# Kernel tuning notes

Hardware: AMD Instinct MI355X
Metric: run time of the kernel (lower is better)

## Reference

```python
import jax, jax.numpy as jnp
import numpy as np

QUERY_DIM = 1024
KEY_DIM = 768
NUM_HEADS = 16
HEAD_DIM = QUERY_DIM // NUM_HEADS
SCALE = HEAD_DIM ** -0.5


def setup_inputs() -> dict:
    key = jax.random.key(0)
    ks = jax.random.split(key, 11)
    B, Nq, Nk = 4, 4096, 1024
    s_q = QUERY_DIM ** -0.5
    s_k = KEY_DIM ** -0.5
    return {
        "query": jax.random.normal(ks[0], (B, Nq, QUERY_DIM), jnp.float32),
        "key": jax.random.normal(ks[1], (B, Nk, KEY_DIM), jnp.float32),
        "value": jax.random.normal(ks[2], (B, Nk, KEY_DIM), jnp.float32),
        "Wq": jax.random.normal(ks[3], (QUERY_DIM, QUERY_DIM), jnp.float32) * s_q,
        "bq": jnp.zeros((QUERY_DIM,), jnp.float32),
        "Wk": jax.random.normal(ks[4], (KEY_DIM, QUERY_DIM), jnp.float32) * s_k,
        "bk": jnp.zeros((QUERY_DIM,), jnp.float32),
        "Wv": jax.random.normal(ks[5], (KEY_DIM, QUERY_DIM), jnp.float32) * s_k,
        "bv": jnp.zeros((QUERY_DIM,), jnp.float32),
        "Wo": jax.random.normal(ks[6], (QUERY_DIM, QUERY_DIM), jnp.float32) * s_q,
        "bo": jnp.zeros((QUERY_DIM,), jnp.float32),
    }


def reference(query, key, value, Wq, bq, Wk, bk, Wv, bv, Wo, bo):
    B, Nq, _ = query.shape
    Nk = key.shape[1]
    # projections to (B, H, N, d)
    q = (query @ Wq + bq).reshape(B, Nq, NUM_HEADS, HEAD_DIM).transpose(0, 2, 1, 3)
    k = (key @ Wk + bk).reshape(B, Nk, NUM_HEADS, HEAD_DIM).transpose(0, 2, 1, 3)
    v = (value @ Wv + bv).reshape(B, Nk, NUM_HEADS, HEAD_DIM).transpose(0, 2, 1, 3)
    attn = jnp.einsum("bhqd,bhkd->bhqk", q, k) * SCALE
    attn = jax.nn.softmax(attn, axis=-1)
    out = jnp.einsum("bhqk,bhkd->bhqd", attn, v)
    out = out.transpose(0, 2, 1, 3).reshape(B, Nq, QUERY_DIM)
    return out @ Wo + bo
```

## Files before the change

### kernel.cpp

```cpp
#include <hip/hip_runtime.h>
#include <hip/hip_bf16.h>
#include <stdint.h>


typedef unsigned short u16;
typedef __attribute__((ext_vector_type(8))) short short8;
typedef __attribute__((ext_vector_type(4))) float f32x4;

#define B_SZ 4
#define NQ   4096
#define NK   1024
#define QDIM 1024
#define KDIM 768
#define NH   16
#define HD   64
#define QSCALE (0.125f * 1.44269504f)

__device__ __forceinline__ u16 f2bf(float f) {
  union { float f; uint32_t u; } v; v.f = f;
  uint32_t u = v.u;
  return (u16)((u + 0x7FFFu + ((u >> 16) & 1u)) >> 16);
}

__device__ __forceinline__ uint32_t pk2(float a, float b) {
  union { __hip_bfloat162 h; uint32_t u; } cv;
  cv.h = __float22bfloat162_rn(float2{a, b});
  return cv.u;
}

__device__ __forceinline__ float fexp2(float x) {
  return __builtin_amdgcn_exp2f(x);
}

__device__ __forceinline__ void async16(u16* lds, const u16* g) {
  __builtin_amdgcn_global_load_lds(
      (__attribute__((address_space(1))) void*)(g),
      (__attribute__((address_space(3))) void*)(lds), 16, 0, 0);
}

__global__ __launch_bounds__(256) void f32_to_bf16_k(const float* __restrict__ in,
                                                     u16* __restrict__ out, int n4) {
  int i = blockIdx.x * 256 + threadIdx.x;
  if (i < n4) {
    f32x4 v = ((const f32x4*)in)[i];
    uint2 o = {pk2(v.x, v.y), pk2(v.z, v.w)};
    ((uint2*)out)[i] = o;
  }
}

__global__ __launch_bounds__(256) void f32_to_bf16_2k(const float* __restrict__ a,
                                                      const float* __restrict__ b,
                                                      u16* __restrict__ oa,
                                                      u16* __restrict__ ob, int n4) {
  int i = blockIdx.x * 256 + threadIdx.x;
  const float* in = blockIdx.y ? b : a;
  u16* out = blockIdx.y ? ob : oa;
  if (i < n4) {
    f32x4 v = ((const f32x4*)in)[i];
    uint2 o = {pk2(v.x, v.y), pk2(v.z, v.w)};
    ((uint2*)out)[i] = o;
  }
}

__global__ __launch_bounds__(256) void transpose_bf16_k(const float* __restrict__ W,
                                                        u16* __restrict__ Wt,
                                                        int K, int N) {
  __shared__ float t[32][33];
  int tx = threadIdx.x & 31, ty = threadIdx.x >> 5;
  int nb = blockIdx.x * 32, kb = blockIdx.y * 32;
#pragma unroll
  for (int i = 0; i < 4; ++i)
    t[ty + i * 8][tx] = W[(size_t)(kb + ty + i * 8) * N + nb + tx];
  __syncthreads();
#pragma unroll
  for (int i = 0; i < 4; ++i)
    Wt[(size_t)(nb + ty + i * 8) * K + kb + tx] = f2bf(t[tx][ty + i * 8]);
}

__global__ __launch_bounds__(256) void gemm_bt(const u16* __restrict__ A,
                                               const u16* __restrict__ Bt,
                                               const float* __restrict__ bias,
                                               float* __restrict__ Cf,
                                               u16* __restrict__ Cb,
                                               int M, int N, int K, int out_bf16,
                                               float scale) {
  __shared__ __align__(16) u16 Al[128 * 64];
  __shared__ __align__(16) u16 Bl[128 * 64];
  const int tid = threadIdx.x;
  const int w = tid >> 6, lane = tid & 63;
  const int g = lane >> 4, l15 = lane & 15;
  const int sw = l15 & 7;
  const int mbase = blockIdx.x * 128, nbase = blockIdx.y * 128;
  const int wm = (w & 1) * 64, wn = (w >> 1) * 64;

  f32x4 zero4 = {0.f, 0.f, 0.f, 0.f};
  f32x4 acc[4][4];
#pragma unroll
  for (int i = 0; i < 4; ++i)
#pragma unroll
    for (int j = 0; j < 4; ++j) acc[i][j] = zero4;

  for (int kb = 0; kb < K; kb += 64) {
#pragma unroll
    for (int i = 0; i < 4; ++i) {
      int cbase = w * 256 + i * 64;
      int c = cbase + lane;
      int row = c >> 3;
      int kc8 = ((c & 7) ^ (row & 7)) * 8;
      async16(&Al[cbase * 8], A + (size_t)(mbase + row) * K + kb + kc8);
      async16(&Bl[cbase * 8], Bt + (size_t)(nbase + row) * K + kb + kc8);
    }
    __syncthreads();
#pragma unroll
    for (int ks = 0; ks < 2; ++ks) {
      short8 af[4], bf[4];
#pragma unroll
      for (int mt = 0; mt < 4; ++mt)
        af[mt] = *(const short8*)&Al[(wm + mt * 16 + l15) * 64 + ((ks * 4 + g) ^ sw) * 8];
#pragma unroll
      for (int nt = 0; nt < 4; ++nt)
        bf[nt] = *(const short8*)&Bl[(wn + nt * 16 + l15) * 64 + ((ks * 4 + g) ^ sw) * 8];
#pragma unroll
      for (int mt = 0; mt < 4; ++mt)
#pragma unroll
        for (int nt = 0; nt < 4; ++nt)
          acc[mt][nt] = __builtin_amdgcn_mfma_f32_16x16x32_bf16(af[mt], bf[nt],
                                                                acc[mt][nt], 0, 0, 0);
    }
    __syncthreads();
  }

#pragma unroll
  for (int nt = 0; nt < 4; ++nt) {
    int col = nbase + wn + nt * 16 + l15;
    float bv = bias[col];
#pragma unroll
    for (int mt = 0; mt < 4; ++mt)
#pragma unroll
      for (int r = 0; r < 4; ++r) {
        int row = mbase + wm + mt * 16 + g * 4 + r;
        float v = (acc[mt][nt][r] + bv) * scale;
        if (out_bf16) Cb[(size_t)row * N + col] = f2bf(v);
        else          Cf[(size_t)row * N + col] = v;
      }
  }
}

__global__ __launch_bounds__(256) void gemm_kv(const u16* __restrict__ kA,
                                               const u16* __restrict__ vA,
                                               const u16* __restrict__ Wk,
                                               const u16* __restrict__ Wv,
                                               const float* __restrict__ bk,
                                               const float* __restrict__ bv,
                                               u16* __restrict__ Kp,
                                               u16* __restrict__ VT,
                                               int M, int N, int K) {
  __shared__ __align__(16) u16 Al[128 * 64];
  __shared__ __align__(16) u16 Bl[128 * 64];
  const int ct = blockIdx.z;
  const u16* A  = ct ? vA : kA;
  const u16* Bt = ct ? Wv : Wk;
  const float* bias = ct ? bv : bk;
  const int tid = threadIdx.x;
  const int w = tid >> 6, lane = tid & 63;
  const int g = lane >> 4, l15 = lane & 15;
  const int sw = l15 & 7;
  const int mbase = blockIdx.x * 128, nbase = blockIdx.y * 128;
  const int wm = (w & 1) * 64, wn = (w >> 1) * 64;

  f32x4 zero4 = {0.f, 0.f, 0.f, 0.f};
  f32x4 acc[4][4];
#pragma unroll
  for (int i = 0; i < 4; ++i)
#pragma unroll
    for (int j = 0; j < 4; ++j) acc[i][j] = zero4;

  for (int kb = 0; kb < K; kb += 64) {
#pragma unroll
    for (int i = 0; i < 4; ++i) {
      int cbase = w * 256 + i * 64;
      int c = cbase + lane;
      int row = c >> 3;
      int kc8 = ((c & 7) ^ (row & 7)) * 8;
      async16(&Al[cbase * 8], A + (size_t)(mbase + row) * K + kb + kc8);
      async16(&Bl[cbase * 8], Bt + (size_t)(nbase + row) * K + kb + kc8);
    }
    __syncthreads();
#pragma unroll
    for (int ks = 0; ks < 2; ++ks) {
      short8 af[4], bf[4];
#pragma unroll
      for (int mt = 0; mt < 4; ++mt)
        af[mt] = *(const short8*)&Al[(wm + mt * 16 + l15) * 64 + ((ks * 4 + g) ^ sw) * 8];
#pragma unroll
      for (int nt = 0; nt < 4; ++nt)
        bf[nt] = *(const short8*)&Bl[(wn + nt * 16 + l15) * 64 + ((ks * 4 + g) ^ sw) * 8];
      if (ct) {
#pragma unroll
        for (int nt = 0; nt < 4; ++nt)
#pragma unroll
          for (int mt = 0; mt < 4; ++mt)
            acc[nt][mt] = __builtin_amdgcn_mfma_f32_16x16x32_bf16(bf[nt], af[mt],
                                                                  acc[nt][mt], 0, 0, 0);
      } else {
#pragma unroll
        for (int mt = 0; mt < 4; ++mt)
#pragma unroll
          for (int nt = 0; nt < 4; ++nt)
            acc[mt][nt] = __builtin_amdgcn_mfma_f32_16x16x32_bf16(af[mt], bf[nt],
                                                                  acc[mt][nt], 0, 0, 0);
      }
    }
    __syncthreads();
  }

  if (ct) {
#pragma unroll
    for (int mt = 0; mt < 4; ++mt) {
      int m = mbase + wm + mt * 16 + l15;
#pragma unroll
      for (int nt = 0; nt < 4; ++nt)
#pragma unroll
        for (int r = 0; r < 4; ++r) {
          int n = nbase + wn + nt * 16 + g * 4 + r;
          VT[(size_t)n * M + m] = f2bf(acc[nt][mt][r] + bias[n]);
        }
    }
  } else {
#pragma unroll
    for (int nt = 0; nt < 4; ++nt) {
      int col = nbase + wn + nt * 16 + l15;
      float bvv = bias[col];
#pragma unroll
      for (int mt = 0; mt < 4; ++mt)
#pragma unroll
        for (int r = 0; r < 4; ++r) {
          int row = mbase + wm + mt * 16 + g * 4 + r;
          Kp[(size_t)row * N + col] = f2bf(acc[mt][nt][r] + bvv);
        }
    }
  }
}

__global__ __launch_bounds__(256, 2) void attn_kernel(const u16* __restrict__ Qp,
                                                      const u16* __restrict__ Kp,
                                                      const u16* __restrict__ VT,
                                                      u16* __restrict__ AO) {
  __shared__ __align__(16) u16 K_lds[2][64 * 64];
  __shared__ __align__(16) u16 V_lds[3][64 * 64];
  __shared__ __align__(16) u16 P_lds[4][32 * 64];

  const int tid = threadIdx.x;
  const int w = tid >> 6, lane = tid & 63;
  const int g = lane >> 4, l15 = lane & 15;
  const int sw = l15 & 7;
  const int bh = blockIdx.y, b = bh >> 4, h = bh & 15;
  const int qrow0 = blockIdx.x * 128 + w * 32;
  const int MT = B_SZ * NK;

  const int cbase0 = (w * 2 + 0) * 64;
  const int cbase1 = (w * 2 + 1) * 64;
  const int c0 = cbase0 + lane, c1 = cbase1 + lane;
  const int row0 = c0 >> 3, kc80 = ((c0 & 7) ^ (row0 & 7)) * 8;
  const int row1 = c1 >> 3, kc81 = ((c1 & 7) ^ (row1 & 7)) * 8;

  const u16* kp0 = Kp + (size_t)(b * NK + row0) * QDIM + h * HD + kc80;
  const u16* kp1 = Kp + (size_t)(b * NK + row1) * QDIM + h * HD + kc81;
  const u16* vp0 = VT + (size_t)(h * HD + row0) * MT + b * NK + kc80;
  const u16* vp1 = VT + (size_t)(h * HD + row1) * MT + b * NK + kc81;

  const int rb = l15 * 64;
  const int cs0 = (g ^ sw) * 8;
  const int cs1 = ((4 + g) ^ sw) * 8;
  const int pwb = rb + (((g >> 1) ^ (sw & 1)) * 8) + (g & 1) * 4;
  const int pms = sw & 6;

  short8 ones8;
#pragma unroll
  for (int j = 0; j < 8; ++j) ones8[j] = (short)0x3F80;

  short8 qf[2][2];
#pragma unroll
  for (int qt = 0; qt < 2; ++qt)
#pragma unroll
    for (int ks = 0; ks < 2; ++ks) {
      size_t row = (size_t)(b * NQ + qrow0 + qt * 16 + l15);
      qf[qt][ks] = *(const short8*)(Qp + row * QDIM + h * HD + ks * 32 + g * 8);
    }

  f32x4 zero4 = {0.f, 0.f, 0.f, 0.f};
  f32x4 o4[4][2];
  f32x4 lacc[2];
#pragma unroll
  for (int dt = 0; dt < 4; ++dt)
#pragma unroll
    for (int qt = 0; qt < 2; ++qt) o4[dt][qt] = zero4;
  lacc[0] = zero4; lacc[1] = zero4;

  u16* Pl = &P_lds[w][0];

  async16(&K_lds[0][cbase0 * 8], kp0);
  async16(&K_lds[0][cbase1 * 8], kp1);
  async16(&V_lds[0][cbase0 * 8], vp0);
  async16(&V_lds[0][cbase1 * 8], vp1);
  kp0 += 64 * QDIM; kp1 += 64 * QDIM; vp0 += 64; vp1 += 64;
  __syncthreads();

  async16(&K_lds[1][cbase0 * 8], kp0);
  async16(&K_lds[1][cbase1 * 8], kp1);
  async16(&V_lds[1][cbase0 * 8], vp0);
  async16(&V_lds[1][cbase1 * 8], vp1);
  kp0 += 64 * QDIM; kp1 += 64 * QDIM; vp0 += 64; vp1 += 64;

  {
    const u16* Kl = &K_lds[0][0];
    f32x4 sc[4][2];
    short8 kf0[4], kf1[4];
#pragma unroll
    for (int mt = 0; mt < 4; ++mt) {
      kf0[mt] = *(const short8*)&Kl[mt * 1024 + rb + cs0];
      kf1[mt] = *(const short8*)&Kl[mt * 1024 + rb + cs1];
    }
    __builtin_amdgcn_s_setprio(1);
#pragma unroll
    for (int mt = 0; mt < 4; ++mt)
#pragma unroll
      for (int qt = 0; qt < 2; ++qt)
        sc[mt][qt] = __builtin_amdgcn_mfma_f32_16x16x32_bf16(kf0[mt], qf[qt][0],
                                                             zero4, 0, 0, 0);
#pragma unroll
    for (int mt = 0; mt < 4; ++mt)
#pragma unroll
      for (int qt = 0; qt < 2; ++qt)
        sc[mt][qt] = __builtin_amdgcn_mfma_f32_16x16x32_bf16(kf1[mt], qf[qt][1],
                                                             sc[mt][qt], 0, 0, 0);
    __builtin_amdgcn_s_setprio(0);
#pragma unroll
    for (int qt = 0; qt < 2; ++qt)
#pragma unroll
      for (int mt = 0; mt < 4; ++mt) {
        float p0 = fexp2(sc[mt][qt][0]);
        float p1 = fexp2(sc[mt][qt][1]);
        float p2 = fexp2(sc[mt][qt][2]);
        float p3 = fexp2(sc[mt][qt][3]);
        uint2 pk = {pk2(p0, p1), pk2(p2, p3)};
        *(uint2*)&Pl[qt * 1024 + pwb + ((mt * 2) ^ pms) * 8] = pk;
      }
  }
  __syncthreads();

  for (int kc = 1; kc < NK / 64; ++kc) {
    const int pv = (kc - 1) % 3;
    if (kc + 1 < NK / 64) {
      const int nk = (kc + 1) & 1, nv = (kc + 1) % 3;
      async16(&K_lds[nk][cbase0 * 8], kp0);
      async16(&K_lds[nk][cbase1 * 8], kp1);
      async16(&V_lds[nv][cbase0 * 8], vp0);
      async16(&V_lds[nv][cbase1 * 8], vp1);
      kp0 += 64 * QDIM; kp1 += 64 * QDIM; vp0 += 64; vp1 += 64;
    }
    const u16* Kl = &K_lds[kc & 1][0];
    const u16* Vl = &V_lds[pv][0];

    short8 pb[2][2], vf[2][4], kf[2][4];
#pragma unroll
    for (int qt = 0; qt < 2; ++qt) {
      pb[0][qt] = *(const short8*)&Pl[qt * 1024 + rb + cs0];
      pb[1][qt] = *(const short8*)&Pl[qt * 1024 + rb + cs1];
    }
#pragma unroll
    for (int dt = 0; dt < 4; ++dt) {
      vf[0][dt] = *(const short8*)&Vl[dt * 1024 + rb + cs0];
      vf[1][dt] = *(const short8*)&Vl[dt * 1024 + rb + cs1];
    }
#pragma unroll
    for (int mt = 0; mt < 4; ++mt) {
      kf[0][mt] = *(const short8*)&Kl[mt * 1024 + rb + cs0];
      kf[1][mt] = *(const short8*)&Kl[mt * 1024 + rb + cs1];
    }

    f32x4 sc[4][2];
    __builtin_amdgcn_s_setprio(1);
#pragma unroll
    for (int mt = 0; mt < 4; ++mt)
#pragma unroll
      for (int qt = 0; qt < 2; ++qt)
        sc[mt][qt] = __builtin_amdgcn_mfma_f32_16x16x32_bf16(kf[0][mt], qf[qt][0],
                                                             zero4, 0, 0, 0);
#pragma unroll
    for (int qt = 0; qt < 2; ++qt)
      lacc[qt] = __builtin_amdgcn_mfma_f32_16x16x32_bf16(ones8, pb[0][qt],
                                                         lacc[qt], 0, 0, 0);
#pragma unroll
    for (int dt = 0; dt < 4; ++dt)
#pragma unroll
      for (int qt = 0; qt < 2; ++qt)
        o4[dt][qt] = __builtin_amdgcn_mfma_f32_16x16x32_bf16(vf[0][dt], pb[0][qt],
                                                             o4[dt][qt], 0, 0, 0);
#pragma unroll
    for (int mt = 0; mt < 4; ++mt)
#pragma unroll
      for (int qt = 0; qt < 2; ++qt)
        sc[mt][qt] = __builtin_amdgcn_mfma_f32_16x16x32_bf16(kf[1][mt], qf[qt][1],
                                                             sc[mt][qt], 0, 0, 0);
#pragma unroll
    for (int qt = 0; qt < 2; ++qt)
      lacc[qt] = __builtin_amdgcn_mfma_f32_16x16x32_bf16(ones8, pb[1][qt],
                                                         lacc[qt], 0, 0, 0);
#pragma unroll
    for (int dt = 0; dt < 4; ++dt)
#pragma unroll
      for (int qt = 0; qt < 2; ++qt)
        o4[dt][qt] = __builtin_amdgcn_mfma_f32_16x16x32_bf16(vf[1][dt], pb[1][qt],
                                                             o4[dt][qt], 0, 0, 0);
    __builtin_amdgcn_s_setprio(0);

#pragma unroll
    for (int qt = 0; qt < 2; ++qt)
#pragma unroll
      for (int mt = 0; mt < 4; ++mt) {
        float p0 = fexp2(sc[mt][qt][0]);
        float p1 = fexp2(sc[mt][qt][1]);
        float p2 = fexp2(sc[mt][qt][2]);
        float p3 = fexp2(sc[mt][qt][3]);
        uint2 pk = {pk2(p0, p1), pk2(p2, p3)};
        *(uint2*)&Pl[qt * 1024 + pwb + ((mt * 2) ^ pms) * 8] = pk;
      }

    asm volatile("s_waitcnt vmcnt(2)" ::: "memory");
    __builtin_amdgcn_sched_barrier(0);
    __builtin_amdgcn_s_barrier();
  }

  asm volatile("s_waitcnt vmcnt(0)" ::: "memory");
  __builtin_amdgcn_sched_barrier(0);
  __builtin_amdgcn_s_barrier();

  {
    const u16* Vl = &V_lds[(NK / 64 - 1) % 3][0];
    short8 pb[2][2], vf[2][4];
#pragma unroll
    for (int qt = 0; qt < 2; ++qt) {
      pb[0][qt] = *(const short8*)&Pl[qt * 1024 + rb + cs0];
      pb[1][qt] = *(const short8*)&Pl[qt * 1024 + rb + cs1];
    }
#pragma unroll
    for (int dt = 0; dt < 4; ++dt) {
      vf[0][dt] = *(const short8*)&Vl[dt * 1024 + rb + cs0];
      vf[1][dt] = *(const short8*)&Vl[dt * 1024 + rb + cs1];
    }
    __builtin_amdgcn_s_setprio(1);
#pragma unroll
    for (int ks = 0; ks < 2; ++ks) {
#pragma unroll
      for (int qt = 0; qt < 2; ++qt)
        lacc[qt] = __builtin_amdgcn_mfma_f32_16x16x32_bf16(ones8, pb[ks][qt],
                                                           lacc[qt], 0, 0, 0);
#pragma unroll
      for (int dt = 0; dt < 4; ++dt)
#pragma unroll
        for (int qt = 0; qt < 2; ++qt)
          o4[dt][qt] = __builtin_amdgcn_mfma_f32_16x16x32_bf16(vf[ks][dt], pb[ks][qt],
                                                               o4[dt][qt], 0, 0, 0);
    }
    __builtin_amdgcn_s_setprio(0);
  }

#pragma unroll
  for (int qt = 0; qt < 2; ++qt) {
    float inv = __builtin_amdgcn_rcpf(lacc[qt][0]);
    size_t row = (size_t)(b * NQ + qrow0 + qt * 16 + l15);
#pragma unroll
    for (int dt = 0; dt < 4; ++dt) {
      uint2 pk = {pk2(o4[dt][qt][0] * inv, o4[dt][qt][1] * inv),
                  pk2(o4[dt][qt][2] * inv, o4[dt][qt][3] * inv)};
      *(uint2*)(AO + row * QDIM + h * HD + dt * 16 + g * 4) = pk;
    }
  }
}

extern "C" void kernel_launch(void* const* d_in, const int* in_sizes, int n_in,
                              void* d_out, int out_size, void* d_ws, size_t ws_size,
                              hipStream_t stream) {
  const float* query = (const float*)d_in[0];
  const float* key   = (const float*)d_in[1];
  const float* value = (const float*)d_in[2];
  const float* Wq = (const float*)d_in[3];
  const float* bq = (const float*)d_in[4];
  const float* Wk = (const float*)d_in[5];
  const float* bk = (const float*)d_in[6];
  const float* Wv = (const float*)d_in[7];
  const float* bv = (const float*)d_in[8];
  const float* Wo = (const float*)d_in[9];
  const float* bo = (const float*)d_in[10];

  char* ws = (char*)d_ws;
  size_t off = 0;
  auto alloc = [&](size_t bytes) -> void* {
    void* p = ws + off;
    off += (bytes + 255) & ~(size_t)255;
    return p;
  };
  const size_t NQTOT = (size_t)B_SZ * NQ;
  const size_t NKTOT = (size_t)B_SZ * NK;
  u16* qbf = (u16*)alloc(NQTOT * QDIM * 2);
  u16* kbf = (u16*)alloc(NKTOT * KDIM * 2);
  u16* vbf = (u16*)alloc(NKTOT * KDIM * 2);
  u16* wqt = (u16*)alloc((size_t)QDIM * QDIM * 2);
  u16* wkt = (u16*)alloc((size_t)KDIM * QDIM * 2);
  u16* wvt = (u16*)alloc((size_t)KDIM * QDIM * 2);
  u16* wot = (u16*)alloc((size_t)QDIM * QDIM * 2);
  u16* Qp  = (u16*)alloc(NQTOT * QDIM * 2);
  u16* Kp  = (u16*)alloc(NKTOT * QDIM * 2);
  u16* VT  = (u16*)alloc((size_t)QDIM * NKTOT * 2);
  u16* AO  = qbf;

  {
    int n4 = (int)(NQTOT * QDIM / 4);
    f32_to_bf16_k<<<(n4 + 255) / 256, 256, 0, stream>>>(query, qbf, n4);
  }
  {
    int n4 = (int)(NKTOT * KDIM / 4);
    f32_to_bf16_2k<<<dim3((n4 + 255) / 256, 2), 256, 0, stream>>>(key, value, kbf,
                                                                  vbf, n4);
  }
  transpose_bf16_k<<<dim3(QDIM / 32, QDIM / 32), 256, 0, stream>>>(Wq, wqt, QDIM, QDIM);
  transpose_bf16_k<<<dim3(QDIM / 32, KDIM / 32), 256, 0, stream>>>(Wk, wkt, KDIM, QDIM);
  transpose_bf16_k<<<dim3(QDIM / 32, KDIM / 32), 256, 0, stream>>>(Wv, wvt, KDIM, QDIM);
  transpose_bf16_k<<<dim3(QDIM / 32, QDIM / 32), 256, 0, stream>>>(Wo, wot, QDIM, QDIM);

  gemm_bt<<<dim3(NQTOT / 128, QDIM / 128), 256, 0, stream>>>(
      qbf, wqt, bq, nullptr, Qp, (int)NQTOT, QDIM, QDIM, 1, QSCALE);
  gemm_kv<<<dim3(NKTOT / 128, QDIM / 128, 2), 256, 0, stream>>>(
      kbf, vbf, wkt, wvt, bk, bv, Kp, VT, (int)NKTOT, QDIM, KDIM);

  attn_kernel<<<dim3(NQ / 128, B_SZ * NH), 256, 0, stream>>>(Qp, Kp, VT, AO);

  gemm_bt<<<dim3(NQTOT / 128, QDIM / 128), 256, 0, stream>>>(
      AO, wot, bo, (float*)d_out, nullptr, (int)NQTOT, QDIM, QDIM, 0, 1.0f);

  (void)in_sizes; (void)n_in; (void)out_size; (void)ws_size;
}
```

Before: 422.0 us.

## Use 128x256 tiles with triple-buffered async loads in Q/O projection GEMMs

Replaces the 128x128, 256-thread GEMM with a 512-thread kernel computing 128x256 tiles. It uses a three-stage LDS ring buffer with async global-to-LDS prefetch two tiles ahead. Each k-step is split into two MFMA halves interleaved with loads, explicit waitcnt/barriers and setprio. The aim is to hide global load latency and raise B-tile reuse, at the cost of higher LDS use per block (144 KB for two blocks) and more complex synchronization.

Result: no change. 415.4 us (-1.6%).

```diff
diff --git a/kernel.cpp b/kernel.cpp
--- a/kernel.cpp
+++ b/kernel.cpp
@@ -77,21 +77,39 @@
     Wt[(size_t)(nb + ty + i * 8) * K + kb + tx] = f2bf(t[tx][ty + i * 8]);
 }
 
-__global__ __launch_bounds__(256) void gemm_bt(const u16* __restrict__ A,
-                                               const u16* __restrict__ Bt,
-                                               const float* __restrict__ bias,
-                                               float* __restrict__ Cf,
-                                               u16* __restrict__ Cb,
-                                               int M, int N, int K, int out_bf16,
-                                               float scale) {
-  __shared__ __align__(16) u16 Al[128 * 64];
-  __shared__ __align__(16) u16 Bl[128 * 64];
+__global__ __launch_bounds__(512, 2) void gemm_bt256(const u16* __restrict__ A,
+                                                     const u16* __restrict__ Bt,
+                                                     const float* __restrict__ bias,
+                                                     float* __restrict__ Cf,
+                                                     u16* __restrict__ Cb,
+                                                     int M, int N, int K,
+                                                     int out_bf16, float scale) {
+  __shared__ __align__(16) u16 Al[3][128 * 64];
+  __shared__ __align__(16) u16 Bl[3][256 * 64];
   const int tid = threadIdx.x;
   const int w = tid >> 6, lane = tid & 63;
   const int g = lane >> 4, l15 = lane & 15;
   const int sw = l15 & 7;
-  const int mbase = blockIdx.x * 128, nbase = blockIdx.y * 128;
+  const int mbase = blockIdx.x * 128, nbase = blockIdx.y * 256;
   const int wm = (w & 1) * 64, wn = (w >> 1) * 64;
+  const int NT = K >> 6;
+
+  const int ca0 = 0 * 512 + tid, ca1 = 1 * 512 + tid;
+  const int ra0 = ca0 >> 3, rc0 = ((ca0 & 7) ^ (ra0 & 7)) * 8;
+  const int ra1 = ca1 >> 3, rc1 = ((ca1 & 7) ^ (ra1 & 7)) * 8;
+  const u16* pa0 = A + (size_t)(mbase + ra0) * K + rc0;
+  const u16* pa1 = A + (size_t)(mbase + ra1) * K + rc1;
+  const u16* pb[4];
+#pragma unroll
+  for (int i = 0; i < 4; ++i) {
+    int c = i * 512 + tid;
+    int row = c >> 3, col = ((c & 7) ^ (row & 7)) * 8;
+    pb[i] = Bt + (size_t)(nbase + row) * K + col;
+  }
+  const int lA0 = (0 * 512 + w * 64) * 8, lA1 = (1 * 512 + w * 64) * 8;
+  int lB[4];
+#pragma unroll
+  for (int i = 0; i < 4; ++i) lB[i] = (i * 512 + w * 64) * 8;
 
   f32x4 zero4 = {0.f, 0.f, 0.f, 0.f};
   f32x4 acc[4][4];
@@ -100,34 +118,96 @@
 #pragma unroll
     for (int j = 0; j < 4; ++j) acc[i][j] = zero4;
 
-  for (int kb = 0; kb < K; kb += 64) {
-#pragma unroll
-    for (int i = 0; i < 4; ++i) {
-      int cbase = w * 256 + i * 64;
-      int c = cbase + lane;
-      int row = c >> 3;
-      int kc8 = ((c & 7) ^ (row & 7)) * 8;
-      async16(&Al[cbase * 8], A + (size_t)(mbase + row) * K + kb + kc8);
-      async16(&Bl[cbase * 8], Bt + (size_t)(nbase + row) * K + kb + kc8);
-    }
-    __syncthreads();
-#pragma unroll
-    for (int ks = 0; ks < 2; ++ks) {
-      short8 af[4], bf[4];
+  async16(&Al[0][lA0], pa0); async16(&Al[0][lA1], pa1);
+#pragma unroll
+  for (int i = 0; i < 4; ++i) async16(&Bl[0][lB[i]], pb[i]);
+  pa0 += 64; pa1 += 64;
+#pragma unroll
+  for (int i = 0; i < 4; ++i) pb[i] += 64;
+  async16(&Al[1][lA0], pa0); async16(&Al[1][lA1], pa1);
+#pragma unroll
+  for (int i = 0; i < 4; ++i) async16(&Bl[1][lB[i]], pb[i]);
+  pa0 += 64; pa1 += 64;
+#pragma unroll
+  for (int i = 0; i < 4; ++i) pb[i] += 64;
+  asm volatile("s_waitcnt vmcnt(6)" ::: "memory");
+  __builtin_amdgcn_sched_barrier(0);
+  __builtin_amdgcn_s_barrier();
+
+  int cb = 0, sb = 2;
+  for (int kt = 0; kt < NT; ++kt) {
+    const u16* Ap = &Al[cb][0];
+    const u16* Bp = &Bl[cb][0];
+    const bool st = (kt + 2 < NT);
+
+    short8 af[4][2], bfa[2][2];
+#pragma unroll
+    for (int mt = 0; mt < 4; ++mt) {
+      af[mt][0] = *(const short8*)&Ap[(wm + mt * 16 + l15) * 64 + (g ^ sw) * 8];
+      af[mt][1] = *(const short8*)&Ap[(wm + mt * 16 + l15) * 64 + ((4 + g) ^ sw) * 8];
+    }
+#pragma unroll
+    for (int nt = 0; nt < 2; ++nt) {
+      bfa[nt][0] = *(const short8*)&Bp[(wn + nt * 16 + l15) * 64 + (g ^ sw) * 8];
+      bfa[nt][1] = *(const short8*)&Bp[(wn + nt * 16 + l15) * 64 + ((4 + g) ^ sw) * 8];
+    }
+    if (st) {
+      async16(&Al[sb][lA0], pa0);
+      async16(&Al[sb][lA1], pa1);
+      async16(&Bl[sb][lB[0]], pb[0]);
+      async16(&Bl[sb][lB[1]], pb[1]);
+    }
+    __builtin_amdgcn_s_barrier();
+    asm volatile("s_waitcnt lgkmcnt(0)" ::: "memory");
+    __builtin_amdgcn_sched_barrier(0);
+    __builtin_amdgcn_s_setprio(1);
+#pragma unroll
+    for (int ks = 0; ks < 2; ++ks)
 #pragma unroll
       for (int mt = 0; mt < 4; ++mt)
-        af[mt] = *(const short8*)&Al[(wm + mt * 16 + l15) * 64 + ((ks * 4 + g) ^ sw) * 8];
-#pragma unroll
-      for (int nt = 0; nt < 4; ++nt)
-        bf[nt] = *(const short8*)&Bl[(wn + nt * 16 + l15) * 64 + ((ks * 4 + g) ^ sw) * 8];
+#pragma unroll
+        for (int nt = 0; nt < 2; ++nt)
+          acc[mt][nt] = __builtin_amdgcn_mfma_f32_16x16x32_bf16(af[mt][ks], bfa[nt][ks],
+                                                                acc[mt][nt], 0, 0, 0);
+    __builtin_amdgcn_s_setprio(0);
+    __builtin_amdgcn_s_barrier();
+
+    short8 bfb[2][2];
+#pragma unroll
+    for (int nt = 0; nt < 2; ++nt) {
+      bfb[nt][0] = *(const short8*)&Bp[(wn + (nt + 2) * 16 + l15) * 64 + (g ^ sw) * 8];
+      bfb[nt][1] = *(const short8*)&Bp[(wn + (nt + 2) * 16 + l15) * 64 + ((4 + g) ^ sw) * 8];
+    }
+    if (st) {
+      async16(&Bl[sb][lB[2]], pb[2]);
+      async16(&Bl[sb][lB[3]], pb[3]);
+      pa0 += 64; pa1 += 64;
+#pragma unroll
+      for (int i = 0; i < 4; ++i) pb[i] += 64;
+    }
+    __builtin_amdgcn_s_barrier();
+    asm volatile("s_waitcnt lgkmcnt(0)" ::: "memory");
+    __builtin_amdgcn_sched_barrier(0);
+    __builtin_amdgcn_s_setprio(1);
+#pragma unroll
+    for (int ks = 0; ks < 2; ++ks)
 #pragma unroll
       for (int mt = 0; mt < 4; ++mt)
 #pragma unroll
-        for (int nt = 0; nt < 4; ++nt)
-          acc[mt][nt] = __builtin_amdgcn_mfma_f32_16x16x32_bf16(af[mt], bf[nt],
-                                                                acc[mt][nt], 0, 0, 0);
-    }
-    __syncthreads();
+        for (int nt = 0; nt < 2; ++nt)
+          acc[mt][nt + 2] = __builtin_amdgcn_mfma_f32_16x16x32_bf16(af[mt][ks], bfb[nt][ks],
+                                                                    acc[mt][nt + 2], 0, 0, 0);
+    __builtin_amdgcn_s_setprio(0);
+
+    if (kt < NT - 2) {
+      asm volatile("s_waitcnt vmcnt(6)" ::: "memory");
+    } else if (kt == NT - 2) {
+      asm volatile("s_waitcnt vmcnt(0)" ::: "memory");
+    }
+    __builtin_amdgcn_sched_barrier(0);
+    __builtin_amdgcn_s_barrier();
+    cb = (cb == 2) ? 0 : cb + 1;
+    sb = (sb == 2) ? 0 : sb + 1;
   }
 
 #pragma unroll
@@ -529,14 +609,14 @@
   transpose_bf16_k<<<dim3(QDIM / 32, KDIM / 32), 256, 0, stream>>>(Wv, wvt, KDIM, QDIM);
   transpose_bf16_k<<<dim3(QDIM / 32, QDIM / 32), 256, 0, stream>>>(Wo, wot, QDIM, QDIM);
 
-  gemm_bt<<<dim3(NQTOT / 128, QDIM / 128), 256, 0, stream>>>(
+  gemm_bt256<<<dim3(NQTOT / 128, QDIM / 256), 512, 0, stream>>>(
       qbf, wqt, bq, nullptr, Qp, (int)NQTOT, QDIM, QDIM, 1, QSCALE);
   gemm_kv<<<dim3(NKTOT / 128, QDIM / 128, 2), 256, 0, stream>>>(
       kbf, vbf, wkt, wvt, bk, bv, Kp, VT, (int)NKTOT, QDIM, KDIM);
 
   attn_kernel<<<dim3(NQ / 128, B_SZ * NH), 256, 0, stream>>>(Qp, Kp, VT, AO);
 
-  gemm_bt<<<dim3(NQTOT / 128, QDIM / 128), 256, 0, stream>>>(
+  gemm_bt256<<<dim3(NQTOT / 128, QDIM / 256), 512, 0, stream>>>(
       AO, wot, bo, (float*)d_out, nullptr, (int)NQTOT, QDIM, QDIM, 0, 1.0f);
 
   (void)in_sizes; (void)n_in; (void)out_size; (void)ws_size;
```
